# Kernel optimization log

Measured on AMD Instinct MI355X. Metric: run time of the kernel, lower is better.

The kernel has to match this reference:

```python
import jax, jax.numpy as jnp
import numpy as np

EMB = 768
HEADS = 8

def setup_inputs() -> dict:
    key = jax.random.key(0)
    ks = jax.random.split(key, 9)
    B, N, E = 16, 1024, EMB
    s = 1.0 / np.sqrt(E)
    x = jax.random.normal(ks[0], (B, N, E), dtype=jnp.float32)
    Wq = jax.random.normal(ks[1], (E, E), dtype=jnp.float32) * s
    bq = jnp.zeros((E,), dtype=jnp.float32)
    Wk = jax.random.normal(ks[2], (E, E), dtype=jnp.float32) * s
    bk = jnp.zeros((E,), dtype=jnp.float32)
    Wv = jax.random.normal(ks[3], (E, E), dtype=jnp.float32) * s
    bv = jnp.zeros((E,), dtype=jnp.float32)
    Wo = jax.random.normal(ks[4], (E, E), dtype=jnp.float32) * s
    bo = jnp.zeros((E,), dtype=jnp.float32)
    return {"x": x, "Wq": Wq, "bq": bq, "Wk": Wk, "bk": bk, "Wv": Wv, "bv": bv, "Wo": Wo, "bo": bo}

def reference(x, Wq, bq, Wk, bk, Wv, bv, Wo, bo):
    B, N, E = x.shape
    H = HEADS
    D = E // H
    # separate Q/K/V linears, split heads: b n (h d) -> b h n d
    q = (x @ Wq + bq).reshape(B, N, H, D).transpose(0, 2, 1, 3)
    k = (x @ Wk + bk).reshape(B, N, H, D).transpose(0, 2, 1, 3)
    v = (x @ Wv + bv).reshape(B, N, H, D).transpose(0, 2, 1, 3)
    energy = jnp.einsum('bhqd,bhkd->bhqk', q, k)
    # NON-STANDARD: softmax first, then divide by sqrt(emb_size)
    scaling = jnp.float32(E) ** 0.5
    attn = jax.nn.softmax(energy, axis=-1) / scaling
    out = jnp.einsum('bhqk,bhkd->bhqd', attn, v)
    out = out.transpose(0, 2, 1, 3).reshape(B, N, E)  # b h n d -> b n (h d)
    return out @ Wo + bo
```

## Files before the change

kernel.cpp:

```cpp
#include <hip/hip_runtime.h>


typedef _Float16 half8 __attribute__((ext_vector_type(8)));
typedef __fp16 fp16x2 __attribute__((ext_vector_type(2)));
typedef float f32x4 __attribute__((ext_vector_type(4)));

__device__ __forceinline__ void gload_lds16(const void* g, void* l) {
  __builtin_amdgcn_global_load_lds((const __attribute__((address_space(1))) void*)g,
                                   (__attribute__((address_space(3))) void*)l, 16, 0, 0);
}


__global__ __launch_bounds__(256) void conv_x_kernel(const float* __restrict__ x,
                                                     _Float16* __restrict__ xh) {
  long i = ((long)blockIdx.x * 256 + threadIdx.x) * 8;
  float4 a = *(const float4*)(x + i);
  float4 b = *(const float4*)(x + i + 4);
  half8 o;
  o[0] = (_Float16)a.x; o[1] = (_Float16)a.y; o[2] = (_Float16)a.z; o[3] = (_Float16)a.w;
  o[4] = (_Float16)b.x; o[5] = (_Float16)b.y; o[6] = (_Float16)b.z; o[7] = (_Float16)b.w;
  *(half8*)(xh + i) = o;
}

__global__ __launch_bounds__(256) void transpose_cvt_kernel(
    const float* __restrict__ W0, const float* __restrict__ W1,
    const float* __restrict__ W2, const float* __restrict__ W3,
    _Float16* __restrict__ WT) {
  __shared__ float tile[32][33];
  int z = blockIdx.z;
  const float* W = (z == 0) ? W0 : (z == 1) ? W1 : (z == 2) ? W2 : W3;
  int k0 = blockIdx.y * 32, n0 = blockIdx.x * 32;
  int tx = threadIdx.x, ty = threadIdx.y;
#pragma unroll
  for (int j = ty; j < 32; j += 8)
    tile[j][tx] = W[(size_t)(k0 + j) * 768 + n0 + tx];
  __syncthreads();
  _Float16* dst = WT + (size_t)z * 768 * 768;
#pragma unroll
  for (int j = ty; j < 32; j += 8)
    dst[(size_t)(n0 + j) * 768 + k0 + tx] = (_Float16)tile[tx][j];
}

__global__ __launch_bounds__(256) void conv_bias_kernel(const float* __restrict__ bq,
                                                        const float* __restrict__ bk,
                                                        const float* __restrict__ bv,
                                                        float* __restrict__ bias) {
  int i = blockIdx.x * 256 + threadIdx.x;
  if (i >= 2304) return;
  bias[i] = (i < 768) ? bq[i] : (i < 1536) ? bk[i - 768] : bv[i - 1536];
}


template <int OUT_F16>
__global__ __launch_bounds__(256) void gemm_nt_kernel(
    const _Float16* __restrict__ A, const _Float16* __restrict__ Bt,
    const float* __restrict__ bias, void* __restrict__ C,
    int M, int N, int K, int ldc) {
  __shared__ _Float16 As[128 * 32];
  __shared__ _Float16 Bs[128 * 32];
  int nbx = N >> 7;
  int nwg = gridDim.x;
  int wg = blockIdx.x;
  int cpx = nwg >> 3;
  int swz = (wg & 7) * cpx + (wg >> 3);
  int bx = swz % nbx, by = swz / nbx;
  int m0 = by * 128, n0 = bx * 128;
  int t = threadIdx.x, l = t & 63, w = t >> 6;
  int lg = l >> 4, lr = l & 15;
  int wr = w >> 1, wc = w & 1;
  f32x4 acc[4][4] = {};

  for (int k0 = 0; k0 < K; k0 += 32) {
    __syncthreads();
#pragma unroll
    for (int j = 0; j < 2; ++j) {
      int slot = j * 256 + t;
      gload_lds16(A + (size_t)(m0 + (slot >> 2)) * K + k0 + (slot & 3) * 8, &As[slot * 8]);
    }
#pragma unroll
    for (int j = 0; j < 2; ++j) {
      int slot = j * 256 + t;
      gload_lds16(Bt + (size_t)(n0 + (slot >> 2)) * K + k0 + (slot & 3) * 8, &Bs[slot * 8]);
    }
    __syncthreads();
    half8 af[4], bf[4];
#pragma unroll
    for (int r = 0; r < 4; ++r) af[r] = *(const half8*)&As[(wr * 64 + r * 16 + lr) * 32 + lg * 8];
#pragma unroll
    for (int c = 0; c < 4; ++c) bf[c] = *(const half8*)&Bs[(wc * 64 + c * 16 + lr) * 32 + lg * 8];
#pragma unroll
    for (int r = 0; r < 4; ++r)
#pragma unroll
      for (int c = 0; c < 4; ++c)
        acc[r][c] = __builtin_amdgcn_mfma_f32_16x16x32_f16(af[r], bf[c], acc[r][c], 0, 0, 0);
  }

#pragma unroll
  for (int r = 0; r < 4; ++r)
#pragma unroll
    for (int c = 0; c < 4; ++c) {
      int col = n0 + wc * 64 + c * 16 + lr;
      float bb = bias[col];
#pragma unroll
      for (int i = 0; i < 4; ++i) {
        int row = m0 + wr * 64 + r * 16 + lg * 4 + i;
        float v = acc[r][c][i] + bb;
        if (OUT_F16)
          ((_Float16*)C)[(size_t)row * ldc + col] = (_Float16)v;
        else
          ((float*)C)[(size_t)row * ldc + col] = v;
      }
    }
}


__global__ __launch_bounds__(512) void attn_kernel(const _Float16* __restrict__ QKV,
                                                   _Float16* __restrict__ Oh) {
  int hw = blockIdx.x;
  int lin = (hw & 7) * 128 + (hw >> 3);
  int bh = lin >> 3, qt = lin & 7;
  int b = bh >> 3, h = bh & 7;
  int t = threadIdx.x, w = t >> 6, l = t & 63;
  int lg = l >> 4, lr = l & 15;

  __shared__ _Float16 Ks[2][64 * 128];
  __shared__ _Float16 Vts[2][96 * 64];
  __shared__ _Float16 Ps[8][16 * 64];

  const _Float16* Qb = QKV + (size_t)b * 1024 * 2304 + h * 96;
  const _Float16* Kb = Qb + 768;
  const _Float16* Vb = Qb + 1536;

  half8 qf[3];
  {
    int qrow = qt * 128 + w * 16 + lr;
    const _Float16 s = (_Float16)1.4426950408889634f;
#pragma unroll
    for (int c = 0; c < 3; ++c) {
      qf[c] = *(const half8*)&Qb[(size_t)qrow * 2304 + c * 32 + lg * 8];
#pragma unroll
      for (int e = 0; e < 8; ++e) qf[c][e] = qf[c][e] * s;
    }
  }

  int ksrc[2], kdst[2];
#pragma unroll
  for (int j = 0; j < 2; ++j) {
    int slot = j * 512 + t;
    int kv = slot >> 4, seg = slot & 15;
    ksrc[j] = kv * 2304 + (seg ^ (kv & 7)) * 8;
    kdst[j] = slot * 8;
  }
  bool vact = t < 384;
  int kvp = t / 12, m = t % 12;
  int vsrc = 2 * kvp * 2304 + m * 8;
  int vdst[8];
#pragma unroll
  for (int e = 0; e < 8; ++e) {
    int d = m * 8 + e;
    int sw = ((d & 7) ^ ((d >> 3) & 7)) << 3;
    vdst[e] = d * 64 + ((2 * kvp) ^ sw);
  }
  int swq = (lr & 7) << 3;
  int poff[4];
#pragma unroll
  for (int tt = 0; tt < 4; ++tt) poff[tt] = lr * 64 + ((tt * 16 + lg * 4) ^ swq);

  auto stage = [&](int kv0, int bi) {
    size_t goff = (size_t)kv0 * 2304;
#pragma unroll
    for (int j = 0; j < 2; ++j)
      gload_lds16(Kb + goff + ksrc[j], &Ks[bi][kdst[j]]);
    if (vact) {
      const _Float16* vp = Vb + goff + vsrc;
      half8 v0 = *(const half8*)vp;
      half8 v1 = *(const half8*)(vp + 2304);
#pragma unroll
      for (int e = 0; e < 8; ++e) {
        union { _Float16 h2[2]; unsigned u32; } pk;
        pk.h2[0] = v0[e]; pk.h2[1] = v1[e];
        *(unsigned*)&Vts[bi][vdst[e]] = pk.u32;
      }
    }
  };

  float m_run = -3.0e38f, l_run = 0.f;
  f32x4 o_acc[6] = {};

  stage(0, 0);

  for (int tile = 0; tile < 16; ++tile) {
    int bi = tile & 1;
    __syncthreads();
    if (tile + 1 < 16) stage((tile + 1) * 64, bi ^ 1);

    f32x4 s_acc[4];
#pragma unroll
    for (int tt = 0; tt < 4; ++tt) {
      s_acc[tt] = f32x4{0.f, 0.f, 0.f, 0.f};
      int kvr = tt * 16 + lr;
#pragma unroll
      for (int c = 0; c < 3; ++c) {
        half8 kf = *(const half8*)&Ks[bi][kvr * 128 + ((c * 4 + lg) ^ (kvr & 7)) * 8];
        s_acc[tt] = __builtin_amdgcn_mfma_f32_16x16x32_f16(kf, qf[c], s_acc[tt], 0, 0, 0);
      }
    }

    float tmax = -3.0e38f;
#pragma unroll
    for (int tt = 0; tt < 4; ++tt)
#pragma unroll
      for (int i = 0; i < 4; ++i) tmax = fmaxf(tmax, s_acc[tt][i]);
    tmax = fmaxf(tmax, __shfl_xor(tmax, 16, 64));
    tmax = fmaxf(tmax, __shfl_xor(tmax, 32, 64));

    if (!__all(tmax <= m_run + 11.5f)) {
      float m_new = fmaxf(m_run, tmax);
      float scale = __builtin_exp2f(m_run - m_new);
      float sc0 = __shfl(scale, lg * 4 + 0, 64);
      float sc1 = __shfl(scale, lg * 4 + 1, 64);
      float sc2 = __shfl(scale, lg * 4 + 2, 64);
      float sc3 = __shfl(scale, lg * 4 + 3, 64);
#pragma unroll
      for (int cc = 0; cc < 6; ++cc) {
        o_acc[cc][0] *= sc0; o_acc[cc][1] *= sc1;
        o_acc[cc][2] *= sc2; o_acc[cc][3] *= sc3;
      }
      l_run *= scale;
      m_run = m_new;
    }

    float rs = 0.f;
#pragma unroll
    for (int tt = 0; tt < 4; ++tt) {
      float p0 = __builtin_exp2f(s_acc[tt][0] - m_run);
      float p1 = __builtin_exp2f(s_acc[tt][1] - m_run);
      float p2 = __builtin_exp2f(s_acc[tt][2] - m_run);
      float p3 = __builtin_exp2f(s_acc[tt][3] - m_run);
      rs += (p0 + p1) + (p2 + p3);
      union { fp16x2 h2[2]; unsigned long long u64; } pk;
      pk.h2[0] = __builtin_amdgcn_cvt_pkrtz(p0, p1);
      pk.h2[1] = __builtin_amdgcn_cvt_pkrtz(p2, p3);
      *(unsigned long long*)&Ps[w][poff[tt]] = pk.u64;
    }
    rs += __shfl_xor(rs, 16, 64);
    rs += __shfl_xor(rs, 32, 64);
    l_run += rs;

#pragma unroll
    for (int kc = 0; kc < 2; ++kc) {
      half8 pf = *(const half8*)&Ps[w][lr * 64 + ((kc * 32 + lg * 8) ^ swq)];
#pragma unroll
      for (int cc = 0; cc < 6; ++cc) {
        int d = cc * 16 + lr;
        int sw = ((d & 7) ^ ((d >> 3) & 7)) << 3;
        half8 vf = *(const half8*)&Vts[bi][d * 64 + ((kc * 32 + lg * 8) ^ sw)];
        o_acc[cc] = __builtin_amdgcn_mfma_f32_16x16x32_f16(pf, vf, o_acc[cc], 0, 0, 0);
      }
    }
  }

  float inv = 1.0f / (l_run * 27.712812921102035f);
  float iv0 = __shfl(inv, lg * 4 + 0, 64);
  float iv1 = __shfl(inv, lg * 4 + 1, 64);
  float iv2 = __shfl(inv, lg * 4 + 2, 64);
  float iv3 = __shfl(inv, lg * 4 + 3, 64);
  size_t rbase = (size_t)(b * 1024 + qt * 128 + w * 16) * 768 + h * 96;
#pragma unroll
  for (int cc = 0; cc < 6; ++cc) {
    int col = cc * 16 + lr;
    Oh[rbase + (size_t)(lg * 4 + 0) * 768 + col] = (_Float16)(o_acc[cc][0] * iv0);
    Oh[rbase + (size_t)(lg * 4 + 1) * 768 + col] = (_Float16)(o_acc[cc][1] * iv1);
    Oh[rbase + (size_t)(lg * 4 + 2) * 768 + col] = (_Float16)(o_acc[cc][2] * iv2);
    Oh[rbase + (size_t)(lg * 4 + 3) * 768 + col] = (_Float16)(o_acc[cc][3] * iv3);
  }
}


extern "C" void kernel_launch(void* const* d_in, const int* in_sizes, int n_in,
                              void* d_out, int out_size, void* d_ws, size_t ws_size,
                              hipStream_t stream) {
  const float* x  = (const float*)d_in[0];
  const float* Wq = (const float*)d_in[1];
  const float* bq = (const float*)d_in[2];
  const float* Wk = (const float*)d_in[3];
  const float* bk = (const float*)d_in[4];
  const float* Wv = (const float*)d_in[5];
  const float* bv = (const float*)d_in[6];
  const float* Wo = (const float*)d_in[7];
  const float* bo = (const float*)d_in[8];
  float* out = (float*)d_out;

  char* ws = (char*)d_ws;
  _Float16* WT   = (_Float16*)(ws);
  float*    bias = (float*)(ws + 4718592);
  _Float16* xh   = (_Float16*)(ws + 4751360);
  _Float16* QKV  = (_Float16*)(ws + 29917184);
  _Float16* Oh   = (_Float16*)(ws + 105414656);

  conv_x_kernel<<<6144, 256, 0, stream>>>(x, xh);
  transpose_cvt_kernel<<<dim3(24, 24, 4), dim3(32, 8), 0, stream>>>(Wq, Wk, Wv, Wo, WT);
  conv_bias_kernel<<<9, 256, 0, stream>>>(bq, bk, bv, bias);

  gemm_nt_kernel<1><<<2304, 256, 0, stream>>>(xh, WT, bias, QKV, 16384, 2304, 768, 2304);

  attn_kernel<<<1024, 512, 0, stream>>>(QKV, Oh);

  gemm_nt_kernel<0><<<768, 256, 0, stream>>>(Oh, WT + (size_t)2304 * 768, bo, out,
                                             16384, 768, 768, 768);
}
```

Baseline: 231.8 us.

## Replace GEMM with 256x256 tiles, double-buffered async LDS loads and XOR swizzle

The QKV and output-projection GEMMs move from 128x128x32 tiles with 256 threads to 256x256x64 tiles with 512 threads. Tiles are double-buffered through direct global-to-LDS loads, with a partial vmcnt wait so the next tile's loads overlap the current tile's MFMAs. An XOR swizzle on the LDS layout is meant to avoid bank conflicts. The larger tiles raise arithmetic intensity, but each tile uses 128 KB of LDS and 128 accumulator floats per thread, so occupancy drops. The output GEMM runs only 192 workgroups, which may leave many CUs idle.

Result: no change. 232.5 us (+0.3%).

```diff
diff --git a/kernel.cpp b/kernel.cpp
--- a/kernel.cpp
+++ b/kernel.cpp
@@ -52,59 +52,89 @@
 
 
 template <int OUT_F16>
-__global__ __launch_bounds__(256) void gemm_nt_kernel(
+__global__ __launch_bounds__(512, 2) void gemm256_kernel(
     const _Float16* __restrict__ A, const _Float16* __restrict__ Bt,
     const float* __restrict__ bias, void* __restrict__ C,
     int M, int N, int K, int ldc) {
-  __shared__ _Float16 As[128 * 32];
-  __shared__ _Float16 Bs[128 * 32];
-  int nbx = N >> 7;
-  int nwg = gridDim.x;
-  int wg = blockIdx.x;
+  __shared__ _Float16 As[2][256 * 64];
+  __shared__ _Float16 Bs[2][256 * 64];
+  int nbx = N >> 8;
+  int nwg = gridDim.x, wg = blockIdx.x;
   int cpx = nwg >> 3;
   int swz = (wg & 7) * cpx + (wg >> 3);
   int bx = swz % nbx, by = swz / nbx;
-  int m0 = by * 128, n0 = bx * 128;
+  int m0 = by * 256, n0 = bx * 256;
   int t = threadIdx.x, l = t & 63, w = t >> 6;
   int lg = l >> 4, lr = l & 15;
-  int wr = w >> 1, wc = w & 1;
-  f32x4 acc[4][4] = {};
-
-  for (int k0 = 0; k0 < K; k0 += 32) {
-    __syncthreads();
-#pragma unroll
-    for (int j = 0; j < 2; ++j) {
-      int slot = j * 256 + t;
-      gload_lds16(A + (size_t)(m0 + (slot >> 2)) * K + k0 + (slot & 3) * 8, &As[slot * 8]);
-    }
-#pragma unroll
-    for (int j = 0; j < 2; ++j) {
-      int slot = j * 256 + t;
-      gload_lds16(Bt + (size_t)(n0 + (slot >> 2)) * K + k0 + (slot & 3) * 8, &Bs[slot * 8]);
-    }
-    __syncthreads();
-    half8 af[4], bf[4];
-#pragma unroll
-    for (int r = 0; r < 4; ++r) af[r] = *(const half8*)&As[(wr * 64 + r * 16 + lr) * 32 + lg * 8];
-#pragma unroll
-    for (int c = 0; c < 4; ++c) bf[c] = *(const half8*)&Bs[(wc * 64 + c * 16 + lr) * 32 + lg * 8];
-#pragma unroll
-    for (int r = 0; r < 4; ++r)
-#pragma unroll
-      for (int c = 0; c < 4; ++c)
-        acc[r][c] = __builtin_amdgcn_mfma_f32_16x16x32_f16(af[r], bf[c], acc[r][c], 0, 0, 0);
-  }
-
-#pragma unroll
-  for (int r = 0; r < 4; ++r)
-#pragma unroll
-    for (int c = 0; c < 4; ++c) {
-      int col = n0 + wc * 64 + c * 16 + lr;
+  int wr = w >> 2, wc = w & 3;
+  f32x4 acc[8][4] = {};
+
+  int srow[4], ssc[4];
+#pragma unroll
+  for (int j = 0; j < 4; ++j) {
+    int slot = j * 512 + t;
+    srow[j] = slot >> 3;
+    ssc[j] = ((slot & 7) ^ (srow[j] & 7)) * 8;
+  }
+
+  auto stage = [&](int kt, int bi) {
+    int k0 = kt * 64;
+#pragma unroll
+    for (int j = 0; j < 4; ++j)
+      gload_lds16(A + (size_t)(m0 + srow[j]) * K + k0 + ssc[j], &As[bi][(j * 512 + t) * 8]);
+#pragma unroll
+    for (int j = 0; j < 4; ++j)
+      gload_lds16(Bt + (size_t)(n0 + srow[j]) * K + k0 + ssc[j], &Bs[bi][(j * 512 + t) * 8]);
+  };
+
+  auto compute = [&](int bi) {
+#pragma unroll
+    for (int kk = 0; kk < 2; ++kk) {
+      half8 bf[4];
+#pragma unroll
+      for (int nf = 0; nf < 4; ++nf) {
+        int row = wc * 64 + nf * 16 + lr;
+        bf[nf] = *(const half8*)&Bs[bi][row * 64 + ((kk * 4 + lg) ^ (row & 7)) * 8];
+      }
+#pragma unroll
+      for (int mf = 0; mf < 8; ++mf) {
+        int row = wr * 128 + mf * 16 + lr;
+        half8 af = *(const half8*)&As[bi][row * 64 + ((kk * 4 + lg) ^ (row & 7)) * 8];
+#pragma unroll
+        for (int nf = 0; nf < 4; ++nf)
+          acc[mf][nf] = __builtin_amdgcn_mfma_f32_16x16x32_f16(af, bf[nf], acc[mf][nf], 0, 0, 0);
+      }
+    }
+  };
+
+  int nkt = K >> 6;
+  stage(0, 0);
+  for (int kt = 0; kt < nkt; ++kt) {
+    int bi = kt & 1;
+    if (kt + 1 < nkt) {
+      stage(kt + 1, bi ^ 1);
+      asm volatile("s_waitcnt vmcnt(8)" ::: "memory");
+    } else {
+      asm volatile("s_waitcnt vmcnt(0)" ::: "memory");
+    }
+    __builtin_amdgcn_sched_barrier(0);
+    __builtin_amdgcn_s_barrier();
+    __builtin_amdgcn_sched_barrier(0);
+    compute(bi);
+    __builtin_amdgcn_sched_barrier(0);
+    __builtin_amdgcn_s_barrier();
+  }
+
+#pragma unroll
+  for (int mf = 0; mf < 8; ++mf)
+#pragma unroll
+    for (int nf = 0; nf < 4; ++nf) {
+      int col = n0 + wc * 64 + nf * 16 + lr;
       float bb = bias[col];
 #pragma unroll
       for (int i = 0; i < 4; ++i) {
-        int row = m0 + wr * 64 + r * 16 + lg * 4 + i;
-        float v = acc[r][c][i] + bb;
+        int row = m0 + wr * 128 + mf * 16 + lg * 4 + i;
+        float v = acc[mf][nf][i] + bb;
         if (OUT_F16)
           ((_Float16*)C)[(size_t)row * ldc + col] = (_Float16)v;
         else
@@ -302,10 +332,10 @@
   transpose_cvt_kernel<<<dim3(24, 24, 4), dim3(32, 8), 0, stream>>>(Wq, Wk, Wv, Wo, WT);
   conv_bias_kernel<<<9, 256, 0, stream>>>(bq, bk, bv, bias);
 
-  gemm_nt_kernel<1><<<2304, 256, 0, stream>>>(xh, WT, bias, QKV, 16384, 2304, 768, 2304);
+  gemm256_kernel<1><<<576, 512, 0, stream>>>(xh, WT, bias, QKV, 16384, 2304, 768, 2304);
 
   attn_kernel<<<1024, 512, 0, stream>>>(QKV, Oh);
 
-  gemm_nt_kernel<0><<<768, 256, 0, stream>>>(Oh, WT + (size_t)2304 * 768, bo, out,
+  gemm256_kernel<0><<<192, 512, 0, stream>>>(Oh, WT + (size_t)2304 * 768, bo, out,
                                              16384, 768, 768, 768);
 }
```
